# Kernel optimization log

Measured on AMD Instinct MI355X. Metric: run time of the kernel, lower is better.

The kernel has to match this reference:

```python
import jax, jax.numpy as jnp
import numpy as np

T, E, DIM, HID = 8192, 8, 1024, 2048


def setup_inputs() -> dict:
    key = jax.random.key(0)
    k1, k2, k3 = jax.random.split(key, 3)
    x = jax.random.normal(k1, (T, DIM), dtype=jnp.float32)
    w1 = jax.random.normal(k2, (E, HID, DIM), dtype=jnp.float32)
    w2 = jax.random.normal(k3, (E, DIM, HID), dtype=jnp.float32)
    # Tokens are pre-grouped by expert; counts must sum exactly to T.
    num_tokens_per_expert = jnp.full((E,), T // E, dtype=jnp.int32)
    return {"x": x, "w1": w1, "w2": w2, "num_tokens_per_expert": num_tokens_per_expert}


def reference(x, w1, w2, num_tokens_per_expert):
    # Faithful to torch._grouped_mm path: bf16 casts, two ragged grouped GEMMs,
    # result cast back to x.dtype.
    gs = num_tokens_per_expert.astype(jnp.int32)
    xb = x.astype(jnp.bfloat16)                                  # [T, dim]
    w1t = jnp.swapaxes(w1.astype(jnp.bfloat16), -2, -1)          # [E, dim, hid]
    w2t = jnp.swapaxes(w2.astype(jnp.bfloat16), -2, -1)          # [E, hid, dim]
    h = jax.lax.ragged_dot(xb, w1t, gs)                          # [T, hid] bf16
    out = jax.lax.ragged_dot(h, w2t, gs)                         # [T, dim] bf16
    return out.astype(x.dtype)
```

## Files before the change

kernel.cpp:

```cpp
#include <hip/hip_runtime.h>
#include <stdint.h>

#define T_TOK 8192
#define NEXP  8
#define DIMSZ 1024
#define HIDSZ 2048

typedef __attribute__((ext_vector_type(4))) float f32x4;
typedef __attribute__((ext_vector_type(8))) short s16x8;


__device__ __forceinline__ uint16_t f2bf(float f) {
  uint32_t u = __builtin_bit_cast(uint32_t, f);
  u += 0x7fffu + ((u >> 16) & 1u);
  return (uint16_t)(u >> 16);
}

__device__ __forceinline__ uint32_t pkbf(float a, float b) {
  return (uint32_t)f2bf(a) | ((uint32_t)f2bf(b) << 16);
}

__device__ __forceinline__ void cvt_unit(const float* __restrict__ src,
                                         uint16_t* __restrict__ dst, size_t j) {
  const float4* p = (const float4*)src + 4 * j;
  float4 a = p[0], b = p[1], c = p[2], d = p[3];
  uint4 o0, o1;
  o0.x = pkbf(a.x, a.y); o0.y = pkbf(a.z, a.w);
  o0.z = pkbf(b.x, b.y); o0.w = pkbf(b.z, b.w);
  o1.x = pkbf(c.x, c.y); o1.y = pkbf(c.z, c.w);
  o1.z = pkbf(d.x, d.y); o1.w = pkbf(d.z, d.w);
  uint4* q = (uint4*)dst + 2 * j;
  q[0] = o0;
  q[1] = o1;
}

__device__ __forceinline__ void gload_lds16(const uint16_t* g, const uint16_t* lds_base) {
  __builtin_amdgcn_global_load_lds(
      (const __attribute__((address_space(1))) uint32_t*)(uintptr_t)g,
      (__attribute__((address_space(3))) uint32_t*)(uint32_t)(uintptr_t)lds_base,
      16, 0, 0);
}


__global__ void cvt_xw1(const float* __restrict__ x, const float* __restrict__ w1,
                        uint16_t* __restrict__ xb, uint16_t* __restrict__ w1b,
                        const int* __restrict__ counts, int* __restrict__ offs,
                        int* __restrict__ toffs) {
  if (blockIdx.x == 0 && threadIdx.x == 0) {
    int s = 0, ts = 0;
    for (int e = 0; e < NEXP; ++e) {
      offs[e] = s; toffs[e] = ts;
      s += counts[e]; ts += (counts[e] + 127) >> 7;
    }
    offs[NEXP] = s; toffs[NEXP] = ts;
  }
  const int NX = (T_TOK * DIMSZ) / 16;
  const int NW = (NEXP * HIDSZ * DIMSZ) / 16;
  const int total = NX + NW;
  const int stride = gridDim.x * blockDim.x;
  for (int i = blockIdx.x * blockDim.x + threadIdx.x; i < total; i += stride) {
    if (i < NX) cvt_unit(x, xb, i);
    else        cvt_unit(w1, w1b, i - NX);
  }
}

template <bool OUT_BF16>
__global__ __launch_bounds__(256, 4)
void gemm_grouped(const uint16_t* __restrict__ A, const uint16_t* __restrict__ B,
                  void* __restrict__ C, const int* __restrict__ offs,
                  const int* __restrict__ toffs, int N, int K, int lognt,
                  const float* __restrict__ cvt_src, uint16_t* __restrict__ cvt_dst,
                  int ncvt, int cvt_units) {
  __shared__ __align__(16) uint16_t As[128 * 64];
  __shared__ __align__(16) uint16_t Bs[128 * 64];

  const int nb = gridDim.x - ncvt;

  if ((int)blockIdx.x >= nb) {
    const int cb = blockIdx.x - nb;
    const int cstride = ncvt * 256;
    for (int u = cb * 256 + threadIdx.x; u < cvt_units; u += cstride)
      cvt_unit(cvt_src, cvt_dst, u);
    return;
  }

  const int orig = blockIdx.x;
  const int qc = nb >> 3, rc = nb & 7, xcd = orig & 7;
  const int bid = (xcd < rc ? xcd * (qc + 1) : rc * (qc + 1) + (xcd - rc) * qc) + (orig >> 3);

  const int mtg = bid >> lognt;
  const int nt  = bid & ((1 << lognt) - 1);
  if (mtg >= toffs[NEXP]) return;
  int e = 0;
#pragma unroll
  for (int i = 1; i < NEXP; ++i) e += (toffs[i] <= mtg) ? 1 : 0;
  const int mt      = mtg - toffs[e];
  const int m_start = offs[e];
  const int m_count = offs[e + 1] - m_start;
  const int m0      = mt * 128;
  int valid_m = m_count - m0;
  if (valid_m > 128) valid_m = 128;
  const int n0 = nt * 128;

  const int tid  = threadIdx.x;
  const int w    = tid >> 6;
  const int lane = tid & 63;
  const int wm = w & 1, wn = w >> 1;

  const uint16_t* gA = A + (size_t)m_start * K;
  const uint16_t* gB = B + (size_t)e * N * K;

  const uint16_t* ap[4];
  const uint16_t* bp[4];
#pragma unroll
  for (int c = 0; c < 4; ++c) {
    const int r  = w * 32 + c * 8 + (lane >> 3);
    const int q8 = ((lane & 7) ^ ((r >> 1) & 7)) * 8;
    const int ra = (r < valid_m) ? r : (valid_m - 1);
    ap[c] = gA + (size_t)(m0 + ra) * K + q8;
    bp[c] = gB + (size_t)(n0 + r) * K + q8;
  }

  const int fr = lane & 15;
  const int f0 = ((lane >> 4) ^ ((fr >> 1) & 7)) * 8;

  f32x4 acc[4][4];
#pragma unroll
  for (int mi = 0; mi < 4; ++mi)
#pragma unroll
    for (int ni = 0; ni < 4; ++ni) acc[mi][ni] = (f32x4){0.f, 0.f, 0.f, 0.f};

  for (int k0 = 0; k0 < K; k0 += 64) {
    __syncthreads();
#pragma unroll
    for (int c = 0; c < 4; ++c) {
      gload_lds16(ap[c], &As[(w * 32 + c * 8) * 64]);
      gload_lds16(bp[c], &Bs[(w * 32 + c * 8) * 64]);
    }
#pragma unroll
    for (int c = 0; c < 4; ++c) { ap[c] += 64; bp[c] += 64; }
    __syncthreads();

#pragma unroll
    for (int kk = 0; kk < 2; ++kk) {
      const int fk = f0 ^ (kk << 5);
      s16x8 af[4], bf[4];
#pragma unroll
      for (int mi = 0; mi < 4; ++mi)
        af[mi] = *(const s16x8*)&As[(wm * 64 + mi * 16 + fr) * 64 + fk];
#pragma unroll
      for (int ni = 0; ni < 4; ++ni)
        bf[ni] = *(const s16x8*)&Bs[(wn * 64 + ni * 16 + fr) * 64 + fk];
#pragma unroll
      for (int mi = 0; mi < 4; ++mi)
#pragma unroll
        for (int ni = 0; ni < 4; ++ni)
          acc[mi][ni] = __builtin_amdgcn_mfma_f32_16x16x32_bf16(af[mi], bf[ni], acc[mi][ni], 0, 0, 0);
    }
  }

  const int cq = (lane >> 4) * 4;
  const int cc = lane & 15;
#pragma unroll
  for (int mi = 0; mi < 4; ++mi) {
#pragma unroll
    for (int r = 0; r < 4; ++r) {
      const int rt = wm * 64 + mi * 16 + cq + r;
      if (rt < valid_m) {
        const size_t rowoff = (size_t)(m_start + m0 + rt) * N;
#pragma unroll
        for (int ni = 0; ni < 4; ++ni) {
          const int col = n0 + wn * 64 + ni * 16 + cc;
          const float v = acc[mi][ni][r];
          if (OUT_BF16) {
            ((uint16_t*)C)[rowoff + col] = f2bf(v);
          } else {
            const uint32_t b = (uint32_t)f2bf(v) << 16;
            ((float*)C)[rowoff + col] = __builtin_bit_cast(float, b);
          }
        }
      }
    }
  }
}


extern "C" void kernel_launch(void* const* d_in, const int* in_sizes, int n_in,
                              void* d_out, int out_size, void* d_ws, size_t ws_size,
                              hipStream_t stream) {
  const float* x  = (const float*)d_in[0];
  const float* w1 = (const float*)d_in[1];
  const float* w2 = (const float*)d_in[2];
  const int* cnt  = (const int*)d_in[3];
  float* out = (float*)d_out;

  char* ws = (char*)d_ws;
  uint16_t* xb  = (uint16_t*)(ws);
  uint16_t* w1b = (uint16_t*)(ws + 16777216);
  uint16_t* w2b = (uint16_t*)(ws + 50331648);
  uint16_t* h   = (uint16_t*)(ws + 83886080);
  int* offs     = (int*)(ws + 117440512);
  int* toffs    = offs + 9;

  cvt_xw1<<<2048, 256, 0, stream>>>(x, w1, xb, w1b, cnt, offs, toffs);

  const int MAX_MT = T_TOK / 128 + NEXP - 1;
  const int NCVT   = 512;
  const int W2U    = (NEXP * DIMSZ * HIDSZ) / 16;

  gemm_grouped<true><<<MAX_MT * 16 + NCVT, 256, 0, stream>>>(
      xb, w1b, (void*)h, offs, toffs, HIDSZ, DIMSZ, 4, w2, w2b, NCVT, W2U);

  gemm_grouped<false><<<MAX_MT * 8, 256, 0, stream>>>(
      h, w2b, (void*)out, offs, toffs, DIMSZ, HIDSZ, 3, (const float*)nullptr,
      (uint16_t*)nullptr, 0, 0);
}
```

Measured before the change: 280.9 us.

## Double-buffer LDS tiles to overlap global loads with MFMA compute

Splits the shared-memory A/B tiles into two ping-pong buffers so the next K-tile's global-to-LDS loads are issued before computing on the current tile, with one barrier per step instead of two. LDS reads are issued through inline ds_read_b128 with explicit waitcnt and sched_barriers to control ordering. This doubles LDS use to 64KB per block and lowers launch bounds from 4 to 2 blocks per CU, trading occupancy for latency hiding.

```diff
diff --git a/kernel.cpp b/kernel.cpp
--- a/kernel.cpp
+++ b/kernel.cpp
@@ -41,6 +41,14 @@
       16, 0, 0);
 }
 
+__device__ __forceinline__ s16x8 ds_read128(const uint16_t* addr) {
+  s16x8 r;
+  asm volatile("ds_read_b128 %0, %1"
+               : "=v"(r)
+               : "v"((uint32_t)(uintptr_t)addr));
+  return r;
+}
+
 
 __global__ void cvt_xw1(const float* __restrict__ x, const float* __restrict__ w1,
                         uint16_t* __restrict__ xb, uint16_t* __restrict__ w1b,
@@ -65,14 +73,16 @@
 }
 
 template <bool OUT_BF16>
-__global__ __launch_bounds__(256, 4)
+__global__ __launch_bounds__(256, 2)
 void gemm_grouped(const uint16_t* __restrict__ A, const uint16_t* __restrict__ B,
                   void* __restrict__ C, const int* __restrict__ offs,
                   const int* __restrict__ toffs, int N, int K, int lognt,
                   const float* __restrict__ cvt_src, uint16_t* __restrict__ cvt_dst,
                   int ncvt, int cvt_units) {
-  __shared__ __align__(16) uint16_t As[128 * 64];
-  __shared__ __align__(16) uint16_t Bs[128 * 64];
+  __shared__ __align__(16) uint16_t As0[128 * 64];
+  __shared__ __align__(16) uint16_t Bs0[128 * 64];
+  __shared__ __align__(16) uint16_t As1[128 * 64];
+  __shared__ __align__(16) uint16_t Bs1[128 * 64];
 
   const int nb = gridDim.x - ncvt;
 
@@ -130,34 +140,60 @@
 #pragma unroll
     for (int ni = 0; ni < 4; ++ni) acc[mi][ni] = (f32x4){0.f, 0.f, 0.f, 0.f};
 
-  for (int k0 = 0; k0 < K; k0 += 64) {
-    __syncthreads();
-#pragma unroll
-    for (int c = 0; c < 4; ++c) {
-      gload_lds16(ap[c], &As[(w * 32 + c * 8) * 64]);
-      gload_lds16(bp[c], &Bs[(w * 32 + c * 8) * 64]);
-    }
-#pragma unroll
-    for (int c = 0; c < 4; ++c) { ap[c] += 64; bp[c] += 64; }
-    __syncthreads();
-
-#pragma unroll
-    for (int kk = 0; kk < 2; ++kk) {
-      const int fk = f0 ^ (kk << 5);
-      s16x8 af[4], bf[4];
-#pragma unroll
-      for (int mi = 0; mi < 4; ++mi)
-        af[mi] = *(const s16x8*)&As[(wm * 64 + mi * 16 + fr) * 64 + fk];
-#pragma unroll
-      for (int ni = 0; ni < 4; ++ni)
-        bf[ni] = *(const s16x8*)&Bs[(wn * 64 + ni * 16 + fr) * 64 + fk];
-#pragma unroll
-      for (int mi = 0; mi < 4; ++mi)
-#pragma unroll
-        for (int ni = 0; ni < 4; ++ni)
-          acc[mi][ni] = __builtin_amdgcn_mfma_f32_16x16x32_bf16(af[mi], bf[ni], acc[mi][ni], 0, 0, 0);
-    }
-  }
+  const int NT = K >> 6;
+
+#pragma unroll
+  for (int c = 0; c < 4; ++c) {
+    gload_lds16(ap[c], &As0[(w * 32 + c * 8) * 64]);
+    gload_lds16(bp[c], &Bs0[(w * 32 + c * 8) * 64]);
+    ap[c] += 64; bp[c] += 64;
+  }
+  asm volatile("s_waitcnt vmcnt(0)" ::: "memory");
+  __builtin_amdgcn_s_barrier();
+  __builtin_amdgcn_sched_barrier(0);
+
+#define GSTEP(CURA, CURB, NXTA, NXTB, MORE)                                    \
+  {                                                                            \
+    if (MORE) {                                                                \
+      _Pragma("unroll")                                                        \
+      for (int c = 0; c < 4; ++c) {                                            \
+        gload_lds16(ap[c], &NXTA[(w * 32 + c * 8) * 64]);                      \
+        gload_lds16(bp[c], &NXTB[(w * 32 + c * 8) * 64]);                      \
+        ap[c] += 64; bp[c] += 64;                                              \
+      }                                                                        \
+    }                                                                          \
+    __builtin_amdgcn_sched_barrier(0);                                         \
+    _Pragma("unroll")                                                          \
+    for (int kk = 0; kk < 2; ++kk) {                                           \
+      const int fk = f0 ^ (kk << 5);                                           \
+      s16x8 af[4], bf[4];                                                      \
+      _Pragma("unroll")                                                        \
+      for (int mi = 0; mi < 4; ++mi)                                           \
+        af[mi] = ds_read128(&CURA[(wm * 64 + mi * 16 + fr) * 64 + fk]);        \
+      _Pragma("unroll")                                                        \
+      for (int ni = 0; ni < 4; ++ni)                                           \
+        bf[ni] = ds_read128(&CURB[(wn * 64 + ni * 16 + fr) * 64 + fk]);        \
+      asm volatile("s_waitcnt lgkmcnt(0)" ::: "memory");                       \
+      __builtin_amdgcn_sched_barrier(0);                                       \
+      _Pragma("unroll")                                                        \
+      for (int mi = 0; mi < 4; ++mi)                                           \
+        _Pragma("unroll")                                                      \
+        for (int ni = 0; ni < 4; ++ni)                                         \
+          acc[mi][ni] = __builtin_amdgcn_mfma_f32_16x16x32_bf16(               \
+              af[mi], bf[ni], acc[mi][ni], 0, 0, 0);                           \
+    }                                                                          \
+    if (MORE) {                                                                \
+      asm volatile("s_waitcnt vmcnt(0)" ::: "memory");                         \
+      __builtin_amdgcn_s_barrier();                                            \
+      __builtin_amdgcn_sched_barrier(0);                                       \
+    }                                                                          \
+  }
+
+  for (int t = 0; t < NT; t += 2) {
+    GSTEP(As0, Bs0, As1, Bs1, (t + 1 < NT));
+    GSTEP(As1, Bs1, As0, Bs0, (t + 2 < NT));
+  }
+#undef GSTEP
 
   const int cq = (lane >> 4) * 4;
   const int cc = lane & 15;
```

Measured after the change: 280.5 us. About the same (-0.1%).
